# Kernel optimization log

Hardware: AMD Instinct MI355X
Metric: run time of the kernel (lower is better)

## Reference

```python
import jax, jax.numpy as jnp
import numpy as np

HIDDEN = 4096
RANK = 4
DELTA = 1.0
BATCH = 4096


def glorot(key, shape):
    return jax.random.uniform(key, shape, minval=-1.0, maxval=1.0) * jnp.sqrt(2.0 / sum(shape))


def setup_inputs() -> dict:
    key = jax.random.key(0)
    k1, k2, k3, k4, k5, k6 = jax.random.split(key, 6)
    return {
        "h": jax.random.normal(k5, (BATCH, HIDDEN), dtype=jnp.float32),
        "x": jax.random.normal(k6, (BATCH, HIDDEN), dtype=jnp.float32),
        "a_diag": glorot(k1, (HIDDEN,)),
        "p_vec": glorot(k2, (HIDDEN, RANK)),
        "q_vec": glorot(k3, (HIDDEN, RANK)),
        "b_mat": glorot(k4, (HIDDEN, HIDDEN)),
    }


def reference(h, x, a_diag, p_vec, q_vec, b_mat):
    # Per-sample original math: (I + delta*(diag(a) + p q^T)) @ h + delta * b_mat.T @ x
    # Batched (rows of h/x are samples) with the Woodbury-style low-rank form:
    #   A_disc @ h  ->  h + delta*(a*h + (h @ q) @ p^T)
    #   B_disc^T @ x -> delta * (x @ b_mat)
    Ah = h + DELTA * (h * a_diag + (h @ q_vec) @ p_vec.T)  # [B, N]
    Bx = DELTA * (x @ b_mat)                               # [B, N]
    return Ah + Bx
```

## Files before the change

### kernel.cpp

```cpp
#include <hip/hip_runtime.h>
#include <hip/hip_bf16.h>
#include <stdint.h>
#include <stddef.h>

#define HIDDEN 4096
#define BATCH  4096
#define RANK   4

typedef _Float16 f16;
typedef __attribute__((ext_vector_type(8))) _Float16 half8;
typedef __attribute__((ext_vector_type(4))) float f32x4;
typedef __attribute__((ext_vector_type(8))) unsigned short ushort8;

#define ASYNC_COPY16(g, l)                                                     \
  __builtin_amdgcn_global_load_lds(                                            \
      (__attribute__((address_space(1))) void*)(g),                            \
      (__attribute__((address_space(3))) void*)(l), 16, 0, 0)

__global__ void cast_f16_kernel(const float* __restrict__ src, f16* __restrict__ dst) {
  size_t i = ((size_t)blockIdx.x * blockDim.x + threadIdx.x) * 8;
  float4 v0 = *(const float4*)(src + i);
  float4 v1 = *(const float4*)(src + i + 4);
  union { f16 h[8]; ushort8 v; } u;
  u.h[0] = (f16)v0.x; u.h[1] = (f16)v0.y; u.h[2] = (f16)v0.z; u.h[3] = (f16)v0.w;
  u.h[4] = (f16)v1.x; u.h[5] = (f16)v1.y; u.h[6] = (f16)v1.z; u.h[7] = (f16)v1.w;
  *(ushort8*)(dst + i) = u.v;
}

__global__ void transpose_cast_kernel(const float* __restrict__ B, f16* __restrict__ Bt) {
  __shared__ f16 tile[64][80];
  const int t = threadIdx.x;
  const int bx = blockIdx.x;
  const int by = blockIdx.y;
  const int tx = t & 15, ty = t >> 4;
  #pragma unroll
  for (int i = 0; i < 4; i++) {
    int row = ty + i * 16;
    float4 v = *(const float4*)(B + (size_t)(by * 64 + row) * HIDDEN + bx * 64 + tx * 4);
    tile[tx * 4 + 0][row] = (f16)v.x;
    tile[tx * 4 + 1][row] = (f16)v.y;
    tile[tx * 4 + 2][row] = (f16)v.z;
    tile[tx * 4 + 3][row] = (f16)v.w;
  }
  __syncthreads();
  const int wx = t & 7, wy = t >> 3;
  #pragma unroll
  for (int i = 0; i < 2; i++) {
    int n = wy + i * 32;
    ushort8 v = *(ushort8*)&tile[n][wx * 8];
    *(ushort8*)(Bt + (size_t)(bx * 64 + n) * HIDDEN + by * 64 + wx * 8) = v;
  }
}

__global__ void hq_kernel(const float* __restrict__ h, const float* __restrict__ q,
                          float* __restrict__ hq) {
  const int b = blockIdx.x;
  const float* hrow = h + (size_t)b * HIDDEN;
  float a0 = 0.f, a1 = 0.f, a2 = 0.f, a3 = 0.f;
  for (int k = threadIdx.x; k < HIDDEN; k += 256) {
    float hv = hrow[k];
    float4 qv = *(const float4*)(q + (size_t)k * RANK);
    a0 += hv * qv.x; a1 += hv * qv.y; a2 += hv * qv.z; a3 += hv * qv.w;
  }
  #pragma unroll
  for (int off = 32; off; off >>= 1) {
    a0 += __shfl_down(a0, off, 64);
    a1 += __shfl_down(a1, off, 64);
    a2 += __shfl_down(a2, off, 64);
    a3 += __shfl_down(a3, off, 64);
  }
  __shared__ float red[4][4];
  const int wave = threadIdx.x >> 6, lane = threadIdx.x & 63;
  if (lane == 0) { red[wave][0] = a0; red[wave][1] = a1; red[wave][2] = a2; red[wave][3] = a3; }
  __syncthreads();
  if (threadIdx.x < 4) {
    float s = red[0][threadIdx.x] + red[1][threadIdx.x] + red[2][threadIdx.x] + red[3][threadIdx.x];
    hq[(size_t)b * RANK + threadIdx.x] = s;
  }
}

#define BM 128
#define BN 128
#define BK 64

__global__ __launch_bounds__(256) void gemm_fused_kernel(
    const f16* __restrict__ Xb, const f16* __restrict__ Bt,
    const float* __restrict__ h, const float* __restrict__ a_diag,
    const float* __restrict__ p_vec, const float* __restrict__ hq,
    float* __restrict__ out) {
  __shared__ f16 As[BM * BK];
  __shared__ f16 Bs[BN * BK];
  const int tid = threadIdx.x;
  const int bm = blockIdx.x, bn = blockIdx.y;
  const int wave = tid >> 6, lane = tid & 63;
  const int wm = wave & 1, wn = wave >> 1;

  const int srow = tid >> 3;
  const int sseg = (tid & 7) ^ (srow & 7);
  const f16* ag = Xb + (size_t)(bm * BM + srow) * HIDDEN + sseg * 8;
  const f16* bg = Bt + (size_t)(bn * BN + srow) * HIDDEN + sseg * 8;
  char* as_base = (char*)As + wave * 1024;
  char* bs_base = (char*)Bs + wave * 1024;
  const size_t rowblk = (size_t)32 * HIDDEN;

  f32x4 acc[4][4];
  #pragma unroll
  for (int i = 0; i < 4; i++)
    #pragma unroll
    for (int j = 0; j < 4; j++)
      acc[i][j] = (f32x4){0.f, 0.f, 0.f, 0.f};

  const int q = lane >> 4;
  const int fm = lane & 15;
  const int swz = lane & 7;

  for (int k0 = 0; k0 < HIDDEN; k0 += BK) {
    #pragma unroll
    for (int o = 0; o < 4; o++) {
      ASYNC_COPY16(ag + o * rowblk, as_base + o * 4096);
      ASYNC_COPY16(bg + o * rowblk, bs_base + o * 4096);
    }
    ag += BK; bg += BK;
    __syncthreads();

    #pragma unroll
    for (int kk = 0; kk < 2; kk++) {
      const int sa = ((kk << 2) | q) ^ swz;
      half8 af[4], bf[4];
      #pragma unroll
      for (int i = 0; i < 4; i++)
        af[i] = *(const half8*)(As + (wm * 64 + i * 16 + fm) * BK + sa * 8);
      #pragma unroll
      for (int j = 0; j < 4; j++)
        bf[j] = *(const half8*)(Bs + (wn * 64 + j * 16 + fm) * BK + sa * 8);
      #pragma unroll
      for (int i = 0; i < 4; i++)
        #pragma unroll
        for (int j = 0; j < 4; j++)
          acc[i][j] = __builtin_amdgcn_mfma_f32_16x16x32_f16(af[i], bf[j], acc[i][j], 0, 0, 0);
    }
    __syncthreads();
  }

  float ad[4];
  float4 pv[4];
  #pragma unroll
  for (int j = 0; j < 4; j++) {
    const int gn = bn * BN + wn * 64 + j * 16 + fm;
    ad[j] = 1.0f + a_diag[gn];
    pv[j] = *(const float4*)(p_vec + (size_t)gn * RANK);
  }
  #pragma unroll
  for (int i = 0; i < 4; i++) {
    #pragma unroll
    for (int r = 0; r < 4; r++) {
      const size_t gb = (size_t)(bm * BM + wm * 64 + i * 16 + q * 4 + r);
      const float4 hv = *(const float4*)(hq + gb * RANK);
      const size_t rowoff = gb * HIDDEN + bn * BN + wn * 64 + fm;
      #pragma unroll
      for (int j = 0; j < 4; j++) {
        const size_t idx = rowoff + j * 16;
        const float hval = __builtin_nontemporal_load(&h[idx]);
        const float v = acc[i][j][r] + hval * ad[j] +
                        hv.x * pv[j].x + hv.y * pv[j].y + hv.z * pv[j].z + hv.w * pv[j].w;
        __builtin_nontemporal_store(v, &out[idx]);
      }
    }
  }
}

__global__ void gemm_f32_fallback_kernel(const float* __restrict__ x, const float* __restrict__ bmat,
                                         const float* __restrict__ h, const float* __restrict__ a_diag,
                                         const float* __restrict__ p_vec, const float* __restrict__ hq,
                                         float* __restrict__ out) {
  __shared__ float As[16][64];
  __shared__ float Bs[16][68];
  const int t = threadIdx.x;
  const int bx = blockIdx.x, by = blockIdx.y;
  const int tm = t & 15, tn = t >> 4;
  float acc[4][4] = {{0.f}};
  for (int k0 = 0; k0 < HIDDEN; k0 += 16) {
    #pragma unroll
    for (int l = 0; l < 4; l++) {
      int idx = t + l * 256;
      int r = idx >> 4, k = idx & 15;
      As[k][r] = x[(size_t)(by * 64 + r) * HIDDEN + k0 + k];
      int kb = idx >> 6, nb = idx & 63;
      Bs[kb][nb] = bmat[(size_t)(k0 + kb) * HIDDEN + bx * 64 + nb];
    }
    __syncthreads();
    #pragma unroll
    for (int k = 0; k < 16; k++) {
      float av[4], bv[4];
      #pragma unroll
      for (int ii = 0; ii < 4; ii++) av[ii] = As[k][tm * 4 + ii];
      #pragma unroll
      for (int jj = 0; jj < 4; jj++) bv[jj] = Bs[k][tn * 4 + jj];
      #pragma unroll
      for (int ii = 0; ii < 4; ii++)
        #pragma unroll
        for (int jj = 0; jj < 4; jj++)
          acc[ii][jj] += av[ii] * bv[jj];
    }
    __syncthreads();
  }
  #pragma unroll
  for (int jj = 0; jj < 4; jj++) {
    int gn = bx * 64 + tn * 4 + jj;
    float ad = 1.0f + a_diag[gn];
    float4 pv = *(const float4*)(p_vec + (size_t)gn * RANK);
    #pragma unroll
    for (int ii = 0; ii < 4; ii++) {
      size_t gb = (size_t)(by * 64 + tm * 4 + ii);
      float4 hv = *(const float4*)(hq + gb * RANK);
      size_t idx = gb * HIDDEN + gn;
      out[idx] = acc[ii][jj] + h[idx] * ad +
                 hv.x * pv.x + hv.y * pv.y + hv.z * pv.z + hv.w * pv.w;
    }
  }
}

extern "C" void kernel_launch(void* const* d_in, const int* in_sizes, int n_in,
                              void* d_out, int out_size, void* d_ws, size_t ws_size,
                              hipStream_t stream) {
  const float* h      = (const float*)d_in[0];
  const float* x      = (const float*)d_in[1];
  const float* a_diag = (const float*)d_in[2];
  const float* p_vec  = (const float*)d_in[3];
  const float* q_vec  = (const float*)d_in[4];
  const float* b_mat  = (const float*)d_in[5];
  float* out = (float*)d_out;

  const size_t nElem = (size_t)BATCH * HIDDEN;
  const size_t hq_bytes = (size_t)BATCH * RANK * sizeof(float);
  const size_t need = hq_bytes + 2 * nElem * sizeof(f16);

  float* hq = (float*)d_ws;
  hq_kernel<<<BATCH, 256, 0, stream>>>(h, q_vec, hq);

  if (ws_size >= need) {
    f16* Xb = (f16*)((char*)d_ws + hq_bytes);
    f16* Bt = Xb + nElem;
    cast_f16_kernel<<<nElem / 2048, 256, 0, stream>>>(x, Xb);
    transpose_cast_kernel<<<dim3(HIDDEN / 64, HIDDEN / 64), 256, 0, stream>>>(b_mat, Bt);
    gemm_fused_kernel<<<dim3(BATCH / BM, HIDDEN / BN), 256, 0, stream>>>(
        Xb, Bt, h, a_diag, p_vec, hq, out);
  } else {
    gemm_f32_fallback_kernel<<<dim3(HIDDEN / 64, BATCH / 64), 256, 0, stream>>>(
        x, b_mat, h, a_diag, p_vec, hq, out);
  }
}
```

Measured before the change: 379.2 us.

## Use 256x256 double-buffered GEMM tiles with interleaved MFMA scheduling and swizzled transpose

```diff
diff --git a/kernel.cpp b/kernel.cpp
--- a/kernel.cpp
+++ b/kernel.cpp
@@ -28,26 +28,31 @@
 }
 
 __global__ void transpose_cast_kernel(const float* __restrict__ B, f16* __restrict__ Bt) {
-  __shared__ f16 tile[64][80];
+  __shared__ __align__(16) f16 tile[64 * 64];
   const int t = threadIdx.x;
   const int bx = blockIdx.x;
   const int by = blockIdx.y;
   const int tx = t & 15, ty = t >> 4;
   #pragma unroll
   for (int i = 0; i < 4; i++) {
-    int row = ty + i * 16;
-    float4 v = *(const float4*)(B + (size_t)(by * 64 + row) * HIDDEN + bx * 64 + tx * 4);
-    tile[tx * 4 + 0][row] = (f16)v.x;
-    tile[tx * 4 + 1][row] = (f16)v.y;
-    tile[tx * 4 + 2][row] = (f16)v.z;
-    tile[tx * 4 + 3][row] = (f16)v.w;
+    const int k = ty + i * 16;
+    float4 v = *(const float4*)(B + (size_t)(by * 64 + k) * HIDDEN + bx * 64 + tx * 4);
+    f16 hv[4];
+    hv[0] = (f16)v.x; hv[1] = (f16)v.y; hv[2] = (f16)v.z; hv[3] = (f16)v.w;
+    #pragma unroll
+    for (int c = 0; c < 4; c++) {
+      const int n = tx * 4 + c;
+      const int phys = (k >> 3) ^ ((n >> 2) & 7);
+      tile[n * 64 + phys * 8 + (k & 7)] = hv[c];
+    }
   }
   __syncthreads();
   const int wx = t & 7, wy = t >> 3;
   #pragma unroll
   for (int i = 0; i < 2; i++) {
-    int n = wy + i * 32;
-    ushort8 v = *(ushort8*)&tile[n][wx * 8];
+    const int n = wy + i * 32;
+    const int phys = wx ^ ((n >> 2) & 7);
+    ushort8 v = *(ushort8*)&tile[n * 64 + phys * 8];
     *(ushort8*)(Bt + (size_t)(bx * 64 + n) * HIDDEN + by * 64 + wx * 8) = v;
   }
 }
@@ -79,84 +84,144 @@
   }
 }
 
-#define BM 128
-#define BN 128
-#define BK 64
-
-__global__ __launch_bounds__(256) void gemm_fused_kernel(
+#define GBM 256
+#define GBN 256
+#define GBK 64
+
+#define BARRIER()                                   \
+  do {                                              \
+    asm volatile("" ::: "memory");                  \
+    __builtin_amdgcn_s_barrier();                   \
+    asm volatile("" ::: "memory");                  \
+  } while (0)
+
+#define VMWAIT0() asm volatile("s_waitcnt vmcnt(0)" ::: "memory")
+
+#define STAGE_TILE(SBUF)                                                     \
+  do {                                                                       \
+    char* ad_ = (char*)(&As[SBUF][0]) + wave * 1024;                         \
+    char* bd_ = (char*)(&Bs[SBUF][0]) + wave * 1024;                         \
+    ASYNC_COPY16(ag + (size_t)0 * 64 * HIDDEN, ad_ + 0 * 8192);              \
+    ASYNC_COPY16(bg + (size_t)0 * 64 * HIDDEN, bd_ + 0 * 8192);              \
+    ASYNC_COPY16(ag + (size_t)1 * 64 * HIDDEN, ad_ + 1 * 8192);              \
+    ASYNC_COPY16(bg + (size_t)1 * 64 * HIDDEN, bd_ + 1 * 8192);              \
+    ASYNC_COPY16(ag + (size_t)2 * 64 * HIDDEN, ad_ + 2 * 8192);              \
+    ASYNC_COPY16(bg + (size_t)2 * 64 * HIDDEN, bd_ + 2 * 8192);              \
+    ASYNC_COPY16(ag + (size_t)3 * 64 * HIDDEN, ad_ + 3 * 8192);              \
+    ASYNC_COPY16(bg + (size_t)3 * 64 * HIDDEN, bd_ + 3 * 8192);              \
+    ag += GBK; bg += GBK;                                                    \
+  } while (0)
+
+#define LDF(base, R16, SG) (*(const half8*)((base) + (R16) * (16 * GBK) + (SG)))
+
+#define MFMA4(I, AF)                                                                    \
+  acc[I][0] = __builtin_amdgcn_mfma_f32_16x16x32_f16(AF, bf0, acc[I][0], 0, 0, 0);      \
+  acc[I][1] = __builtin_amdgcn_mfma_f32_16x16x32_f16(AF, bf1, acc[I][1], 0, 0, 0);      \
+  acc[I][2] = __builtin_amdgcn_mfma_f32_16x16x32_f16(AF, bf2, acc[I][2], 0, 0, 0);      \
+  acc[I][3] = __builtin_amdgcn_mfma_f32_16x16x32_f16(AF, bf3, acc[I][3], 0, 0, 0);
+
+#define TILE(BUF, SBUF, DO_STAGE)                                            \
+  {                                                                          \
+    const f16* Ab_ = &As[BUF][0] + (wm * 128 + fm) * GBK;                    \
+    const f16* Bb_ = &Bs[BUF][0] + (wn * 64 + fm) * GBK;                     \
+    const int sg0_ = ((0 + q) ^ sw) * 8;                                     \
+    const int sg1_ = ((4 + q) ^ sw) * 8;                                     \
+    half8 a0, a1, a2, a3, bf0, bf1, bf2, bf3;                                \
+                         \
+    a0 = LDF(Ab_, 0, sg0_); a1 = LDF(Ab_, 1, sg0_);                          \
+    a2 = LDF(Ab_, 2, sg0_); a3 = LDF(Ab_, 3, sg0_);                          \
+    bf0 = LDF(Bb_, 0, sg0_); bf1 = LDF(Bb_, 1, sg0_);                        \
+    bf2 = LDF(Bb_, 2, sg0_); bf3 = LDF(Bb_, 3, sg0_);                        \
+    if (DO_STAGE) STAGE_TILE(SBUF);                                          \
+    BARRIER();                                                               \
+    __builtin_amdgcn_s_setprio(1);                                           \
+    MFMA4(0, a0) MFMA4(1, a1) MFMA4(2, a2) MFMA4(3, a3)                      \
+    __builtin_amdgcn_s_setprio(0);                                           \
+    BARRIER();                                                               \
+                              \
+    a0 = LDF(Ab_, 4, sg0_); a1 = LDF(Ab_, 5, sg0_);                          \
+    a2 = LDF(Ab_, 6, sg0_); a3 = LDF(Ab_, 7, sg0_);                          \
+    BARRIER();                                                               \
+    __builtin_amdgcn_s_setprio(1);                                           \
+    MFMA4(4, a0) MFMA4(5, a1) MFMA4(6, a2) MFMA4(7, a3)                      \
+    __builtin_amdgcn_s_setprio(0);                                           \
+    BARRIER();                                                               \
+                                            \
+    a0 = LDF(Ab_, 0, sg1_); a1 = LDF(Ab_, 1, sg1_);                          \
+    a2 = LDF(Ab_, 2, sg1_); a3 = LDF(Ab_, 3, sg1_);                          \
+    bf0 = LDF(Bb_, 0, sg1_); bf1 = LDF(Bb_, 1, sg1_);                        \
+    bf2 = LDF(Bb_, 2, sg1_); bf3 = LDF(Bb_, 3, sg1_);                        \
+    BARRIER();                                                               \
+    __builtin_amdgcn_s_setprio(1);                                           \
+    MFMA4(0, a0) MFMA4(1, a1) MFMA4(2, a2) MFMA4(3, a3)                      \
+    __builtin_amdgcn_s_setprio(0);                                           \
+    BARRIER();                                                               \
+         \
+    a0 = LDF(Ab_, 4, sg1_); a1 = LDF(Ab_, 5, sg1_);                          \
+    a2 = LDF(Ab_, 6, sg1_); a3 = LDF(Ab_, 7, sg1_);                          \
+    BARRIER();                                                               \
+    __builtin_amdgcn_s_setprio(1);                                           \
+    MFMA4(4, a0) MFMA4(5, a1) MFMA4(6, a2) MFMA4(7, a3)                      \
+    __builtin_amdgcn_s_setprio(0);                                           \
+    VMWAIT0();                                                               \
+    BARRIER();                                                               \
+  }
+
+__global__ __launch_bounds__(512, 2) void gemm_fused_kernel(
     const f16* __restrict__ Xb, const f16* __restrict__ Bt,
     const float* __restrict__ h, const float* __restrict__ a_diag,
     const float* __restrict__ p_vec, const float* __restrict__ hq,
     float* __restrict__ out) {
-  __shared__ f16 As[BM * BK];
-  __shared__ f16 Bs[BN * BK];
+  __shared__ __align__(16) f16 As[2][GBM * GBK];
+  __shared__ __align__(16) f16 Bs[2][GBN * GBK];
   const int tid = threadIdx.x;
   const int bm = blockIdx.x, bn = blockIdx.y;
   const int wave = tid >> 6, lane = tid & 63;
-  const int wm = wave & 1, wn = wave >> 1;
+  const int wm = wave >> 2, wn = wave & 3;
 
   const int srow = tid >> 3;
-  const int sseg = (tid & 7) ^ (srow & 7);
-  const f16* ag = Xb + (size_t)(bm * BM + srow) * HIDDEN + sseg * 8;
-  const f16* bg = Bt + (size_t)(bn * BN + srow) * HIDDEN + sseg * 8;
-  char* as_base = (char*)As + wave * 1024;
-  char* bs_base = (char*)Bs + wave * 1024;
-  const size_t rowblk = (size_t)32 * HIDDEN;
-
-  f32x4 acc[4][4];
-  #pragma unroll
-  for (int i = 0; i < 4; i++)
+  const int gseg = (tid & 7) ^ (srow & 7);
+  const f16* ag = Xb + (size_t)(bm * GBM + srow) * HIDDEN + gseg * 8;
+  const f16* bg = Bt + (size_t)(bn * GBN + srow) * HIDDEN + gseg * 8;
+
+  f32x4 acc[8][4];
+  #pragma unroll
+  for (int i = 0; i < 8; i++)
     #pragma unroll
     for (int j = 0; j < 4; j++)
       acc[i][j] = (f32x4){0.f, 0.f, 0.f, 0.f};
 
   const int q = lane >> 4;
   const int fm = lane & 15;
-  const int swz = lane & 7;
-
-  for (int k0 = 0; k0 < HIDDEN; k0 += BK) {
-    #pragma unroll
-    for (int o = 0; o < 4; o++) {
-      ASYNC_COPY16(ag + o * rowblk, as_base + o * 4096);
-      ASYNC_COPY16(bg + o * rowblk, bs_base + o * 4096);
-    }
-    ag += BK; bg += BK;
-    __syncthreads();
-
-    #pragma unroll
-    for (int kk = 0; kk < 2; kk++) {
-      const int sa = ((kk << 2) | q) ^ swz;
-      half8 af[4], bf[4];
-      #pragma unroll
-      for (int i = 0; i < 4; i++)
-        af[i] = *(const half8*)(As + (wm * 64 + i * 16 + fm) * BK + sa * 8);
-      #pragma unroll
-      for (int j = 0; j < 4; j++)
-        bf[j] = *(const half8*)(Bs + (wn * 64 + j * 16 + fm) * BK + sa * 8);
-      #pragma unroll
-      for (int i = 0; i < 4; i++)
-        #pragma unroll
-        for (int j = 0; j < 4; j++)
-          acc[i][j] = __builtin_amdgcn_mfma_f32_16x16x32_f16(af[i], bf[j], acc[i][j], 0, 0, 0);
-    }
-    __syncthreads();
-  }
+  const int sw = fm & 7;
+
+  STAGE_TILE(0);
+  VMWAIT0();
+  BARRIER();
+
+  #pragma unroll 1
+  for (int kt2 = 0; kt2 < 31; ++kt2) {
+    TILE(0, 1, true)
+    TILE(1, 0, true)
+  }
+  TILE(0, 1, true)
+  TILE(1, 0, false)
 
   float ad[4];
   float4 pv[4];
   #pragma unroll
   for (int j = 0; j < 4; j++) {
-    const int gn = bn * BN + wn * 64 + j * 16 + fm;
+    const int gn = bn * GBN + wn * 64 + j * 16 + fm;
     ad[j] = 1.0f + a_diag[gn];
     pv[j] = *(const float4*)(p_vec + (size_t)gn * RANK);
   }
   #pragma unroll
-  for (int i = 0; i < 4; i++) {
+  for (int i = 0; i < 8; i++) {
     #pragma unroll
     for (int r = 0; r < 4; r++) {
-      const size_t gb = (size_t)(bm * BM + wm * 64 + i * 16 + q * 4 + r);
+      const size_t gb = (size_t)(bm * GBM + wm * 128 + i * 16 + q * 4 + r);
       const float4 hv = *(const float4*)(hq + gb * RANK);
-      const size_t rowoff = gb * HIDDEN + bn * BN + wn * 64 + fm;
+      const size_t rowoff = gb * HIDDEN + bn * GBN + wn * 64 + fm;
       #pragma unroll
       for (int j = 0; j < 4; j++) {
         const size_t idx = rowoff + j * 16;
@@ -243,7 +308,7 @@
     f16* Bt = Xb + nElem;
     cast_f16_kernel<<<nElem / 2048, 256, 0, stream>>>(x, Xb);
     transpose_cast_kernel<<<dim3(HIDDEN / 64, HIDDEN / 64), 256, 0, stream>>>(b_mat, Bt);
-    gemm_fused_kernel<<<dim3(BATCH / BM, HIDDEN / BN), 256, 0, stream>>>(
+    gemm_fused_kernel<<<dim3(BATCH / GBM, HIDDEN / GBN), 512, 0, stream>>>(
         Xb, Bt, h, a_diag, p_vec, hq, out);
   } else {
     gemm_f32_fallback_kernel<<<dim3(HIDDEN / 64, BATCH / 64), 256, 0, stream>>>(
```

Result: faster. 370.3 us (-2.3%).
